# Kernel tuning notes

Hardware: AMD Instinct MI355X
Metric: run time of the kernel (lower is better)

## Reference

```python
import jax, jax.numpy as jnp
import numpy as np

B, K, T, C = 4, 8, 2048, 64

def setup_inputs() -> dict:
    key = jax.random.key(0)
    ks = jax.random.split(key, 7)
    return {
        "x": jax.random.normal(ks[0], (B, K, T, C), dtype=jnp.float32),
        "Wq": jax.random.normal(ks[1], (C, C), dtype=jnp.float32) / np.sqrt(C),
        "bq": jax.random.normal(ks[2], (C,), dtype=jnp.float32) * 0.01,
        "Wk": jax.random.normal(ks[3], (C, C), dtype=jnp.float32) / np.sqrt(C),
        "bk": jax.random.normal(ks[4], (C,), dtype=jnp.float32) * 0.01,
        "Wv": jax.random.normal(ks[5], (C, C), dtype=jnp.float32) / np.sqrt(C),
        "bv": jax.random.normal(ks[6], (C,), dtype=jnp.float32) * 0.01,
    }

def reference(x, Wq, bq, Wk, bk, Wv, bv):
    c_dim = x.shape[-1]
    # torch nn.Linear: y = x @ W.T + b
    q = jnp.einsum('bktc,dc->bktd', x, Wq) + bq
    k = jnp.einsum('bktc,dc->bktd', x, Wk) + bk
    v = jnp.einsum('bktc,dc->bktd', x, Wv) + bv
    scores = jnp.einsum('bkic,bkjc->bkij', q, k) / jnp.sqrt(jnp.float32(c_dim))
    attn = jax.nn.softmax(scores, axis=-1)
    out = jnp.einsum('bkij,bkjc->bkic', attn, v)
    return out
```

## Files before the change

### kernel.cpp

```cpp
#include <hip/hip_runtime.h>


#define T_DIM 2048
#define NHEAD 32
#define HSTRIDE (T_DIM * 64)
#define QSCALE 0.18033688011112042f
#define SOFF  8.0f

#define SWZ(row, grp) ((row) * 64 + ((((grp) ^ ((row) & 7)) & 7) * 8))

#define RAW_BARRIER() asm volatile("s_waitcnt lgkmcnt(0)\n\ts_barrier" ::: "memory")

typedef _Float16 h8 __attribute__((ext_vector_type(8)));
typedef _Float16 h4 __attribute__((ext_vector_type(4)));
typedef __fp16   g2 __attribute__((ext_vector_type(2)));
typedef float    f4 __attribute__((ext_vector_type(4)));
typedef float    fv16 __attribute__((ext_vector_type(16)));

union H4U { h4 v; g2 p[2]; };
union H8U { h8 v; h4 h[2]; g2 p[4]; };

#if defined(__has_builtin)
#if __has_builtin(__builtin_amdgcn_exp2f)
#define EXP2(x) __builtin_amdgcn_exp2f(x)
#endif
#endif
#ifndef EXP2
__device__ inline float exp2_raw(float x) {
    float r;
    asm("v_exp_f32 %0, %1" : "=v"(r) : "v"(x));
    return r;
}
#define EXP2(x) exp2_raw(x)
#endif

__device__ inline h4 cvt4(f4 x) {
    H4U u;
    u.p[0] = __builtin_amdgcn_cvt_pkrtz(x[0], x[1]);
    u.p[1] = __builtin_amdgcn_cvt_pkrtz(x[2], x[3]);
    return u.v;
}

__device__ inline h8 cvt8(f4 a, f4 b) {
    H8U r;
    r.h[0] = cvt4(a);
    r.h[1] = cvt4(b);
    return r.v;
}

__device__ inline fv16 splat16(float x) {
    fv16 r;
    #pragma unroll
    for (int i = 0; i < 16; ++i) r[i] = x;
    return r;
}

__global__ __launch_bounds__(256) void qkv_proj_kernel(
    const float* __restrict__ x,
    const float* __restrict__ Wq, const float* __restrict__ bq,
    const float* __restrict__ Wk, const float* __restrict__ bk,
    const float* __restrict__ Wv, const float* __restrict__ bv,
    _Float16* __restrict__ qh, _Float16* __restrict__ khT,
    _Float16* __restrict__ vtT)
{
    __shared__ _Float16 ws[3][64 * 64];
    __shared__ _Float16 ot[64 * 64];
    __shared__ float bsh[3][64];

    const int tid  = threadIdx.x;
    const int row0 = blockIdx.x * 64;
    const int head = blockIdx.x >> 5;
    const int t0   = (blockIdx.x & 31) * 64;

    #pragma unroll
    for (int m = 0; m < 3; ++m) {
        const float* Wm = (m == 0) ? Wq : ((m == 1) ? Wk : Wv);
        const float* bm = (m == 0) ? bq : ((m == 1) ? bk : bv);
        #pragma unroll
        for (int pass = 0; pass < 4; ++pass) {
            const int idx = pass * 1024 + tid * 4;
            const int d = idx >> 6, c = idx & 63;
            f4 wv = *(const f4*)(Wm + idx);
            *(h4*)&ws[m][SWZ(d, c >> 3) + (c & 7)] = cvt4(wv);
        }
        if (tid < 64) bsh[m][tid] = bm[tid];
    }

    const int w    = tid >> 6;
    const int lane = tid & 63;
    const int l15  = lane & 15;
    const int qd   = lane >> 4;

    h8 af[2];
    {
        const float* xp = x + (size_t)(row0 + w * 16 + l15) * 64 + qd * 8;
        #pragma unroll
        for (int ch = 0; ch < 2; ++ch) {
            f4 a0 = *(const f4*)(xp + ch * 32);
            f4 a1 = *(const f4*)(xp + ch * 32 + 4);
            af[ch] = cvt8(a0, a1);
        }
    }
    __syncthreads();

    #pragma unroll
    for (int m = 0; m < 3; ++m) {
        h8 bf[4][2];
        #pragma unroll
        for (int ns = 0; ns < 4; ++ns)
            #pragma unroll
            for (int ch = 0; ch < 2; ++ch)
                bf[ns][ch] = *(const h8*)&ws[m][SWZ(ns * 16 + l15, ch * 4 + qd)];

        f4 acc[4];
        #pragma unroll
        for (int ns = 0; ns < 4; ++ns)
            acc[ns] = (f4){0.f, 0.f, 0.f, 0.f};
        #pragma unroll
        for (int ch = 0; ch < 2; ++ch)
            #pragma unroll
            for (int ns = 0; ns < 4; ++ns)
                acc[ns] = __builtin_amdgcn_mfma_f32_16x16x32_f16(
                    af[ch], bf[ns][ch], acc[ns], 0, 0, 0);

        __syncthreads();
        if (m < 2) {
            #pragma unroll
            for (int ns = 0; ns < 4; ++ns) {
                const int d = ns * 16 + l15;
                const float bias = bsh[m][d];
                #pragma unroll
                for (int r = 0; r < 4; ++r) {
                    const int t = w * 16 + qd * 4 + r;
                    float v = acc[ns][r] + bias;
                    if (m == 0) v *= QSCALE;
                    ot[SWZ(t, d >> 3) + (d & 7)] = (_Float16)v;
                }
            }
            __syncthreads();
            if (m == 0) {
                #pragma unroll
                for (int pass = 0; pass < 2; ++pass) {
                    const int t  = pass * 32 + (tid >> 3);
                    const int c0 = (tid & 7) * 8;
                    *(h8*)&qh[(size_t)(row0 + t) * 64 + c0] =
                        *(const h8*)&ot[SWZ(t, tid & 7)];
                }
            } else {
                #pragma unroll
                for (int pass = 0; pass < 2; ++pass) {
                    const int f   = pass * 2048 + tid * 8;
                    const int kb  = f >> 11;
                    const int cs  = (f >> 9) & 3;
                    const int l   = (f >> 3) & 63;
                    const int p   = l & 31;
                    const int w16 = p & 15;
                    const int sw  = ((w16 & 12) == 4) ? (w16 + 4)
                                  : (((w16 & 12) == 8) ? (w16 - 4) : w16);
                    const int tact = kb * 32 + (p & 16) + sw;
                    const int g8   = cs * 2 + (l >> 5);
                    *(h8*)&khT[(size_t)head * HSTRIDE + (t0 >> 6) * 4096 + f] =
                        *(const h8*)&ot[SWZ(tact, g8)];
                }
            }
        } else {
            #pragma unroll
            for (int ns = 0; ns < 4; ++ns) {
                const int d = ns * 16 + l15;
                const float bias = bsh[2][d];
                const int tl = w * 16 + qd * 4;
                f4 pvf;
                #pragma unroll
                for (int r = 0; r < 4; ++r)
                    pvf[r] = acc[ns][r] + bias;
                *(h4*)&ot[SWZ(d, tl >> 3) + (tl & 7)] = cvt4(pvf);
            }
            __syncthreads();
            #pragma unroll
            for (int pass = 0; pass < 2; ++pass) {
                const int f  = pass * 2048 + tid * 8;
                const int q2 = f >> 9;
                const int b  = q2 >> 1, cc = q2 & 1;
                const int l  = (f >> 3) & 63;
                const int c  = cc * 32 + (l & 31);
                const int tg = b * 2 + (l >> 5);
                *(h8*)&vtT[(size_t)head * HSTRIDE + (t0 >> 6) * 4096 + f] =
                    *(const h8*)&ot[SWZ(c, tg)];
            }
        }
    }
}

__global__ __launch_bounds__(384, 2) void attn_kernel(
    const _Float16* __restrict__ qh, const _Float16* __restrict__ khT,
    const _Float16* __restrict__ vtT, float* __restrict__ out)
{
    __shared__ _Float16 tiles[3][8192];
    const int tid  = threadIdx.x;
    const int w    = tid >> 6;
    const int lane = tid & 63;

    const int bid  = blockIdx.x;
    const int xcd  = bid & 7;
    const int slot = bid >> 3;
    const int head = xcd * 4 + (slot >> 3);
    const int qpart = slot & 7;

    if (w < 4) {
        const int q0  = qpart * 256 + w * 64;
        const int l31 = lane & 31;
        const int lh  = lane >> 5;

        h8 qf[2][4];
        #pragma unroll
        for (int qs = 0; qs < 2; ++qs) {
            const _Float16* qp = qh + (size_t)(head * T_DIM + q0 + qs * 32 + l31) * 64 + lh * 8;
            #pragma unroll
            for (int cs = 0; cs < 4; ++cs)
                qf[qs][cs] = *(const h8*)(qp + cs * 16);
        }

        f4 rs4[2] = {(f4){0.f,0.f,0.f,0.f}, (f4){0.f,0.f,0.f,0.f}};
        fv16 oacc[2][2];
        #pragma unroll
        for (int qs = 0; qs < 2; ++qs)
            #pragma unroll
            for (int cc = 0; cc < 2; ++cc)
                oacc[qs][cc] = splat16(0.f);

        const int ko = lane * 8;
        const _Float16* c0 = &tiles[0][0];
        const _Float16* c1 = &tiles[1][0];
        const _Float16* c2 = &tiles[2][0];

        __syncthreads();

        fv16 st[2][2];
        {
            h8 kf[2][4];
            #pragma unroll
            for (int kb = 0; kb < 2; ++kb)
                #pragma unroll
                for (int cs = 0; cs < 4; ++cs)
                    kf[kb][cs] = *(const h8*)(c0 + kb * 2048 + cs * 512 + ko);
            #pragma unroll
            for (int kb = 0; kb < 2; ++kb)
                #pragma unroll
                for (int qs = 0; qs < 2; ++qs)
                    st[kb][qs] = splat16(-SOFF);
            #pragma unroll
            for (int cs = 0; cs < 4; ++cs)
                #pragma unroll
                for (int kb = 0; kb < 2; ++kb)
                    #pragma unroll
                    for (int qs = 0; qs < 2; ++qs)
                        st[kb][qs] = __builtin_amdgcn_mfma_f32_32x32x16_f16(
                            kf[kb][cs], qf[qs][cs], st[kb][qs], 0, 0, 0);
        }

        for (int it = 0; it < 32; ++it) {
            h8 kf[2][4];
            if (it < 31) {
                #pragma unroll
                for (int kb = 0; kb < 2; ++kb)
                    #pragma unroll
                    for (int cs = 0; cs < 4; ++cs)
                        kf[kb][cs] = *(const h8*)(c1 + kb * 2048 + cs * 512 + ko);
            }
            h8 vf[4][2];
            #pragma unroll
            for (int b = 0; b < 4; ++b)
                #pragma unroll
                for (int cc = 0; cc < 2; ++cc)
                    vf[b][cc] = *(const h8*)(c0 + 4096 + (b * 2 + cc) * 512 + ko);

            #pragma unroll
            for (int qs = 0; qs < 2; ++qs) {
                H8U pa[4];
                #pragma unroll
                for (int kb = 0; kb < 2; ++kb)
                    #pragma unroll
                    for (int g = 0; g < 4; ++g) {
                        f4 p;
                        p[0] = EXP2(st[kb][qs][4 * g + 0]);
                        p[1] = EXP2(st[kb][qs][4 * g + 1]);
                        p[2] = EXP2(st[kb][qs][4 * g + 2]);
                        p[3] = EXP2(st[kb][qs][4 * g + 3]);
                        rs4[qs] += p;
                        const int b = kb * 2 + (g >> 1);
                        pa[b].p[(g & 1) * 2 + 0] = __builtin_amdgcn_cvt_pkrtz(p[0], p[1]);
                        pa[b].p[(g & 1) * 2 + 1] = __builtin_amdgcn_cvt_pkrtz(p[2], p[3]);
                    }
                #pragma unroll
                for (int b = 0; b < 4; ++b)
                    #pragma unroll
                    for (int cc = 0; cc < 2; ++cc)
                        oacc[qs][cc] = __builtin_amdgcn_mfma_f32_32x32x16_f16(
                            pa[b].v, vf[b][cc], oacc[qs][cc], 0, 0, 0);
            }

            if (it < 31) {
                #pragma unroll
                for (int kb = 0; kb < 2; ++kb)
                    #pragma unroll
                    for (int qs = 0; qs < 2; ++qs)
                        st[kb][qs] = splat16(-SOFF);
                #pragma unroll
                for (int cs = 0; cs < 4; ++cs)
                    #pragma unroll
                    for (int kb = 0; kb < 2; ++kb)
                        #pragma unroll
                        for (int qs = 0; qs < 2; ++qs)
                            st[kb][qs] = __builtin_amdgcn_mfma_f32_32x32x16_f16(
                                kf[kb][cs], qf[qs][cs], st[kb][qs], 0, 0, 0);
            }

            const _Float16* tmp = c0; c0 = c1; c1 = c2; c2 = tmp;
            __syncthreads();
        }

        #pragma unroll
        for (int qs = 0; qs < 2; ++qs) {
            float lsum = (rs4[qs][0] + rs4[qs][1]) + (rs4[qs][2] + rs4[qs][3]);
            lsum += __shfl_xor(lsum, 32, 64);
            const float linv = 1.f / lsum;
            #pragma unroll
            for (int r = 0; r < 16; ++r) {
                const int qrow = (r & 3) + 8 * (r >> 2) + 4 * lh;
                const float fac = __shfl(linv, qrow, 64);
                #pragma unroll
                for (int cc = 0; cc < 2; ++cc)
                    out[(size_t)(head * T_DIM + q0 + qs * 32 + qrow) * 64 + cc * 32 + l31] =
                        oacc[qs][cc][r] * fac;
            }
        }
    } else {
        const _Float16* src = ((w == 4) ? khT : vtT) + (size_t)head * HSTRIDE;
        const int off = (w - 4) * 4096;
        _Float16* d0 = &tiles[0][off];
        _Float16* d1 = &tiles[1][off];
        _Float16* d2 = &tiles[2][off];
        const int lo = lane * 8;
        h8 sA[8], sB[8];

        #pragma unroll
        for (int b = 0; b < 8; ++b) sA[b] = *(const h8*)(src + b * 512 + lo);
        #pragma unroll
        for (int b = 0; b < 8; ++b) sB[b] = *(const h8*)(src + 4096 + b * 512 + lo);
        #pragma unroll
        for (int b = 0; b < 8; ++b) *(h8*)(d0 + b * 512 + lo) = sA[b];
        #pragma unroll
        for (int b = 0; b < 8; ++b) *(h8*)(d1 + b * 512 + lo) = sB[b];
        #pragma unroll
        for (int b = 0; b < 8; ++b) sA[b] = *(const h8*)(src + 8192 + b * 512 + lo);
        const _Float16* sp = src + 3 * 4096;
        RAW_BARRIER();

        _Float16* w0 = d2;
        _Float16* w1 = d0;
        _Float16* w2 = d1;

        for (int t2 = 0; t2 < 16; ++t2) {
            if (t2 < 15) {
                #pragma unroll
                for (int b = 0; b < 8; ++b) sB[b] = *(const h8*)(sp + b * 512 + lo);
                sp += 4096;
                #pragma unroll
                for (int b = 0; b < 8; ++b) *(h8*)(w0 + b * 512 + lo) = sA[b];
            }
            RAW_BARRIER();
            { _Float16* t = w0; w0 = w1; w1 = w2; w2 = t; }
            if (t2 < 14) {
                #pragma unroll
                for (int b = 0; b < 8; ++b) sA[b] = *(const h8*)(sp + b * 512 + lo);
                sp += 4096;
            }
            if (t2 < 15) {
                #pragma unroll
                for (int b = 0; b < 8; ++b) *(h8*)(w0 + b * 512 + lo) = sB[b];
            }
            RAW_BARRIER();
            { _Float16* t = w0; w0 = w1; w1 = w2; w2 = t; }
        }
    }
}

extern "C" void kernel_launch(void* const* d_in, const int* in_sizes, int n_in,
                              void* d_out, int out_size, void* d_ws, size_t ws_size,
                              hipStream_t stream)
{
    (void)in_sizes; (void)n_in; (void)out_size; (void)ws_size;
    const float* x  = (const float*)d_in[0];
    const float* Wq = (const float*)d_in[1];
    const float* bq = (const float*)d_in[2];
    const float* Wk = (const float*)d_in[3];
    const float* bk = (const float*)d_in[4];
    const float* Wv = (const float*)d_in[5];
    const float* bv = (const float*)d_in[6];
    float* out = (float*)d_out;

    _Float16* qh  = (_Float16*)d_ws;
    _Float16* khT = qh + (size_t)NHEAD * HSTRIDE;
    _Float16* vtT = khT + (size_t)NHEAD * HSTRIDE;

    hipLaunchKernelGGL(qkv_proj_kernel, dim3(1024), dim3(256), 0, stream,
                       x, Wq, bq, Wk, bk, Wv, bv, qh, khT, vtT);
    hipLaunchKernelGGL(attn_kernel, dim3(256), dim3(384), 0, stream,
                       qh, khT, vtT, out);
}
```

Baseline: 124.9 us.

## Halve attention consumer warps per block, double grid, restructure projection epilogue

The attention kernel now uses 2 consumer warps plus 2 loader warps per block (256 threads) and launches 512 blocks, each covering 128 query rows instead of 256. This spreads the work over more blocks and gives more overlap across the CUs. The cost is that each block streams K/V tiles for half as many queries, which doubles total K/V tile traffic. The inner loop now loads K fragments per key block just before use, which lowers register pressure, and raises wave priority with s_setprio around the MFMA section. The projection kernel issues the x loads before the weight staging, reuses the weight LDS as output staging, and collapses the per-matrix barriers into two.

New measurement: 136.8 us. +9.5%, slower.

```diff
diff --git a/kernel.cpp b/kernel.cpp
--- a/kernel.cpp
+++ b/kernel.cpp
@@ -64,13 +64,27 @@
     _Float16* __restrict__ vtT)
 {
     __shared__ _Float16 ws[3][64 * 64];
-    __shared__ _Float16 ot[64 * 64];
     __shared__ float bsh[3][64];
 
     const int tid  = threadIdx.x;
     const int row0 = blockIdx.x * 64;
     const int head = blockIdx.x >> 5;
     const int t0   = (blockIdx.x & 31) * 64;
+
+    const int w    = tid >> 6;
+    const int lane = tid & 63;
+    const int l15  = lane & 15;
+    const int qd   = lane >> 4;
+
+    f4 xa[2][2];
+    {
+        const float* xp = x + (size_t)(row0 + w * 16 + l15) * 64 + qd * 8;
+        #pragma unroll
+        for (int ch = 0; ch < 2; ++ch) {
+            xa[ch][0] = *(const f4*)(xp + ch * 32);
+            xa[ch][1] = *(const f4*)(xp + ch * 32 + 4);
+        }
+    }
 
     #pragma unroll
     for (int m = 0; m < 3; ++m) {
@@ -86,23 +100,14 @@
         if (tid < 64) bsh[m][tid] = bm[tid];
     }
 
-    const int w    = tid >> 6;
-    const int lane = tid & 63;
-    const int l15  = lane & 15;
-    const int qd   = lane >> 4;
-
     h8 af[2];
-    {
-        const float* xp = x + (size_t)(row0 + w * 16 + l15) * 64 + qd * 8;
-        #pragma unroll
-        for (int ch = 0; ch < 2; ++ch) {
-            f4 a0 = *(const f4*)(xp + ch * 32);
-            f4 a1 = *(const f4*)(xp + ch * 32 + 4);
-            af[ch] = cvt8(a0, a1);
-        }
-    }
+    #pragma unroll
+    for (int ch = 0; ch < 2; ++ch)
+        af[ch] = cvt8(xa[ch][0], xa[ch][1]);
+
     __syncthreads();
 
+    f4 acc[3][4];
     #pragma unroll
     for (int m = 0; m < 3; ++m) {
         h8 bf[4][2];
@@ -111,87 +116,84 @@
             #pragma unroll
             for (int ch = 0; ch < 2; ++ch)
                 bf[ns][ch] = *(const h8*)&ws[m][SWZ(ns * 16 + l15, ch * 4 + qd)];
-
-        f4 acc[4];
         #pragma unroll
         for (int ns = 0; ns < 4; ++ns)
-            acc[ns] = (f4){0.f, 0.f, 0.f, 0.f};
+            acc[m][ns] = (f4){0.f, 0.f, 0.f, 0.f};
         #pragma unroll
         for (int ch = 0; ch < 2; ++ch)
             #pragma unroll
             for (int ns = 0; ns < 4; ++ns)
-                acc[ns] = __builtin_amdgcn_mfma_f32_16x16x32_f16(
-                    af[ch], bf[ns][ch], acc[ns], 0, 0, 0);
-
-        __syncthreads();
-        if (m < 2) {
-            #pragma unroll
-            for (int ns = 0; ns < 4; ++ns) {
-                const int d = ns * 16 + l15;
-                const float bias = bsh[m][d];
-                #pragma unroll
-                for (int r = 0; r < 4; ++r) {
-                    const int t = w * 16 + qd * 4 + r;
-                    float v = acc[ns][r] + bias;
-                    if (m == 0) v *= QSCALE;
-                    ot[SWZ(t, d >> 3) + (d & 7)] = (_Float16)v;
-                }
-            }
-            __syncthreads();
-            if (m == 0) {
-                #pragma unroll
-                for (int pass = 0; pass < 2; ++pass) {
-                    const int t  = pass * 32 + (tid >> 3);
-                    const int c0 = (tid & 7) * 8;
-                    *(h8*)&qh[(size_t)(row0 + t) * 64 + c0] =
-                        *(const h8*)&ot[SWZ(t, tid & 7)];
-                }
-            } else {
-                #pragma unroll
-                for (int pass = 0; pass < 2; ++pass) {
-                    const int f   = pass * 2048 + tid * 8;
-                    const int kb  = f >> 11;
-                    const int cs  = (f >> 9) & 3;
-                    const int l   = (f >> 3) & 63;
-                    const int p   = l & 31;
-                    const int w16 = p & 15;
-                    const int sw  = ((w16 & 12) == 4) ? (w16 + 4)
-                                  : (((w16 & 12) == 8) ? (w16 - 4) : w16);
-                    const int tact = kb * 32 + (p & 16) + sw;
-                    const int g8   = cs * 2 + (l >> 5);
-                    *(h8*)&khT[(size_t)head * HSTRIDE + (t0 >> 6) * 4096 + f] =
-                        *(const h8*)&ot[SWZ(tact, g8)];
-                }
-            }
-        } else {
-            #pragma unroll
-            for (int ns = 0; ns < 4; ++ns) {
-                const int d = ns * 16 + l15;
-                const float bias = bsh[2][d];
-                const int tl = w * 16 + qd * 4;
-                f4 pvf;
-                #pragma unroll
-                for (int r = 0; r < 4; ++r)
-                    pvf[r] = acc[ns][r] + bias;
-                *(h4*)&ot[SWZ(d, tl >> 3) + (tl & 7)] = cvt4(pvf);
-            }
-            __syncthreads();
-            #pragma unroll
-            for (int pass = 0; pass < 2; ++pass) {
-                const int f  = pass * 2048 + tid * 8;
-                const int q2 = f >> 9;
-                const int b  = q2 >> 1, cc = q2 & 1;
-                const int l  = (f >> 3) & 63;
-                const int c  = cc * 32 + (l & 31);
-                const int tg = b * 2 + (l >> 5);
-                *(h8*)&vtT[(size_t)head * HSTRIDE + (t0 >> 6) * 4096 + f] =
-                    *(const h8*)&ot[SWZ(c, tg)];
-            }
-        }
-    }
-}
-
-__global__ __launch_bounds__(384, 2) void attn_kernel(
+                acc[m][ns] = __builtin_amdgcn_mfma_f32_16x16x32_f16(
+                    af[ch], bf[ns][ch], acc[m][ns], 0, 0, 0);
+    }
+
+    __syncthreads();
+
+    #pragma unroll
+    for (int m = 0; m < 2; ++m) {
+        #pragma unroll
+        for (int ns = 0; ns < 4; ++ns) {
+            const int d = ns * 16 + l15;
+            const float bias = bsh[m][d];
+            #pragma unroll
+            for (int r = 0; r < 4; ++r) {
+                const int t = w * 16 + qd * 4 + r;
+                float v = acc[m][ns][r] + bias;
+                if (m == 0) v *= QSCALE;
+                ws[m][SWZ(t, d >> 3) + (d & 7)] = (_Float16)v;
+            }
+        }
+    }
+    #pragma unroll
+    for (int ns = 0; ns < 4; ++ns) {
+        const int d = ns * 16 + l15;
+        const float bias = bsh[2][d];
+        const int tl = w * 16 + qd * 4;
+        f4 pvf;
+        #pragma unroll
+        for (int r = 0; r < 4; ++r)
+            pvf[r] = acc[2][ns][r] + bias;
+        *(h4*)&ws[2][SWZ(d, tl >> 3) + (tl & 7)] = cvt4(pvf);
+    }
+
+    __syncthreads();
+
+    #pragma unroll
+    for (int pass = 0; pass < 2; ++pass) {
+        const int t  = pass * 32 + (tid >> 3);
+        const int c0 = (tid & 7) * 8;
+        *(h8*)&qh[(size_t)(row0 + t) * 64 + c0] =
+            *(const h8*)&ws[0][SWZ(t, tid & 7)];
+    }
+    #pragma unroll
+    for (int pass = 0; pass < 2; ++pass) {
+        const int f   = pass * 2048 + tid * 8;
+        const int kb  = f >> 11;
+        const int cs  = (f >> 9) & 3;
+        const int l   = (f >> 3) & 63;
+        const int p   = l & 31;
+        const int w16 = p & 15;
+        const int sw  = ((w16 & 12) == 4) ? (w16 + 4)
+                      : (((w16 & 12) == 8) ? (w16 - 4) : w16);
+        const int tact = kb * 32 + (p & 16) + sw;
+        const int g8   = cs * 2 + (l >> 5);
+        *(h8*)&khT[(size_t)head * HSTRIDE + (t0 >> 6) * 4096 + f] =
+            *(const h8*)&ws[1][SWZ(tact, g8)];
+    }
+    #pragma unroll
+    for (int pass = 0; pass < 2; ++pass) {
+        const int f  = pass * 2048 + tid * 8;
+        const int q2 = f >> 9;
+        const int b  = q2 >> 1, cc = q2 & 1;
+        const int l  = (f >> 3) & 63;
+        const int c  = cc * 32 + (l & 31);
+        const int tg = b * 2 + (l >> 5);
+        *(h8*)&vtT[(size_t)head * HSTRIDE + (t0 >> 6) * 4096 + f] =
+            *(const h8*)&ws[2][SWZ(c, tg)];
+    }
+}
+
+__global__ __launch_bounds__(256, 2) void attn_kernel(
     const _Float16* __restrict__ qh, const _Float16* __restrict__ khT,
     const _Float16* __restrict__ vtT, float* __restrict__ out)
 {
@@ -203,11 +205,11 @@
     const int bid  = blockIdx.x;
     const int xcd  = bid & 7;
     const int slot = bid >> 3;
-    const int head = xcd * 4 + (slot >> 3);
-    const int qpart = slot & 7;
-
-    if (w < 4) {
-        const int q0  = qpart * 256 + w * 64;
+    const int head = xcd * 4 + (slot >> 4);
+    const int qpart = slot & 15;
+
+    if (w < 2) {
+        const int q0  = qpart * 128 + w * 64;
         const int l31 = lane & 31;
         const int lh  = lane >> 5;
 
@@ -236,37 +238,23 @@
         __syncthreads();
 
         fv16 st[2][2];
-        {
-            h8 kf[2][4];
-            #pragma unroll
-            for (int kb = 0; kb < 2; ++kb)
-                #pragma unroll
-                for (int cs = 0; cs < 4; ++cs)
-                    kf[kb][cs] = *(const h8*)(c0 + kb * 2048 + cs * 512 + ko);
-            #pragma unroll
-            for (int kb = 0; kb < 2; ++kb)
+        #pragma unroll
+        for (int kb = 0; kb < 2; ++kb) {
+            h8 kf[4];
+            #pragma unroll
+            for (int cs = 0; cs < 4; ++cs)
+                kf[cs] = *(const h8*)(c0 + kb * 2048 + cs * 512 + ko);
+            st[kb][0] = splat16(-SOFF);
+            st[kb][1] = splat16(-SOFF);
+            #pragma unroll
+            for (int cs = 0; cs < 4; ++cs)
                 #pragma unroll
                 for (int qs = 0; qs < 2; ++qs)
-                    st[kb][qs] = splat16(-SOFF);
-            #pragma unroll
-            for (int cs = 0; cs < 4; ++cs)
-                #pragma unroll
-                for (int kb = 0; kb < 2; ++kb)
-                    #pragma unroll
-                    for (int qs = 0; qs < 2; ++qs)
-                        st[kb][qs] = __builtin_amdgcn_mfma_f32_32x32x16_f16(
-                            kf[kb][cs], qf[qs][cs], st[kb][qs], 0, 0, 0);
+                    st[kb][qs] = __builtin_amdgcn_mfma_f32_32x32x16_f16(
+                        kf[cs], qf[qs][cs], st[kb][qs], 0, 0, 0);
         }
 
         for (int it = 0; it < 32; ++it) {
-            h8 kf[2][4];
-            if (it < 31) {
-                #pragma unroll
-                for (int kb = 0; kb < 2; ++kb)
-                    #pragma unroll
-                    for (int cs = 0; cs < 4; ++cs)
-                        kf[kb][cs] = *(const h8*)(c1 + kb * 2048 + cs * 512 + ko);
-            }
             h8 vf[4][2];
             #pragma unroll
             for (int b = 0; b < 4; ++b)
@@ -274,11 +262,13 @@
                 for (int cc = 0; cc < 2; ++cc)
                     vf[b][cc] = *(const h8*)(c0 + 4096 + (b * 2 + cc) * 512 + ko);
 
-            #pragma unroll
-            for (int qs = 0; qs < 2; ++qs) {
-                H8U pa[4];
-                #pragma unroll
-                for (int kb = 0; kb < 2; ++kb)
+            __builtin_amdgcn_s_setprio(1);
+
+            #pragma unroll
+            for (int qs = 0; qs < 2; ++qs)
+                #pragma unroll
+                for (int kb = 0; kb < 2; ++kb) {
+                    H8U pa[2];
                     #pragma unroll
                     for (int g = 0; g < 4; ++g) {
                         f4 p;
@@ -287,33 +277,38 @@
                         p[2] = EXP2(st[kb][qs][4 * g + 2]);
                         p[3] = EXP2(st[kb][qs][4 * g + 3]);
                         rs4[qs] += p;
-                        const int b = kb * 2 + (g >> 1);
-                        pa[b].p[(g & 1) * 2 + 0] = __builtin_amdgcn_cvt_pkrtz(p[0], p[1]);
-                        pa[b].p[(g & 1) * 2 + 1] = __builtin_amdgcn_cvt_pkrtz(p[2], p[3]);
+                        pa[g >> 1].p[(g & 1) * 2 + 0] = __builtin_amdgcn_cvt_pkrtz(p[0], p[1]);
+                        pa[g >> 1].p[(g & 1) * 2 + 1] = __builtin_amdgcn_cvt_pkrtz(p[2], p[3]);
                     }
-                #pragma unroll
-                for (int b = 0; b < 4; ++b)
                     #pragma unroll
-                    for (int cc = 0; cc < 2; ++cc)
-                        oacc[qs][cc] = __builtin_amdgcn_mfma_f32_32x32x16_f16(
-                            pa[b].v, vf[b][cc], oacc[qs][cc], 0, 0, 0);
-            }
+                    for (int bl = 0; bl < 2; ++bl) {
+                        const int b = kb * 2 + bl;
+                        #pragma unroll
+                        for (int cc = 0; cc < 2; ++cc)
+                            oacc[qs][cc] = __builtin_amdgcn_mfma_f32_32x32x16_f16(
+                                pa[bl].v, vf[b][cc], oacc[qs][cc], 0, 0, 0);
+                    }
+                }
 
             if (it < 31) {
                 #pragma unroll
-                for (int kb = 0; kb < 2; ++kb)
+                for (int kb = 0; kb < 2; ++kb) {
+                    h8 kf[4];
                     #pragma unroll
-                    for (int qs = 0; qs < 2; ++qs)
-                        st[kb][qs] = splat16(-SOFF);
-                #pragma unroll
-                for (int cs = 0; cs < 4; ++cs)
+                    for (int cs = 0; cs < 4; ++cs)
+                        kf[cs] = *(const h8*)(c1 + kb * 2048 + cs * 512 + ko);
+                    st[kb][0] = splat16(-SOFF);
+                    st[kb][1] = splat16(-SOFF);
                     #pragma unroll
-                    for (int kb = 0; kb < 2; ++kb)
+                    for (int cs = 0; cs < 4; ++cs)
                         #pragma unroll
                         for (int qs = 0; qs < 2; ++qs)
                             st[kb][qs] = __builtin_amdgcn_mfma_f32_32x32x16_f16(
-                                kf[kb][cs], qf[qs][cs], st[kb][qs], 0, 0, 0);
-            }
+                                kf[cs], qf[qs][cs], st[kb][qs], 0, 0, 0);
+                }
+            }
+
+            __builtin_amdgcn_s_setprio(0);
 
             const _Float16* tmp = c0; c0 = c1; c1 = c2; c2 = tmp;
             __syncthreads();
@@ -335,8 +330,8 @@
             }
         }
     } else {
-        const _Float16* src = ((w == 4) ? khT : vtT) + (size_t)head * HSTRIDE;
-        const int off = (w - 4) * 4096;
+        const _Float16* src = ((w == 2) ? khT : vtT) + (size_t)head * HSTRIDE;
+        const int off = (w - 2) * 4096;
         _Float16* d0 = &tiles[0][off];
         _Float16* d1 = &tiles[1][off];
         _Float16* d2 = &tiles[2][off];
@@ -405,6 +400,6 @@
 
     hipLaunchKernelGGL(qkv_proj_kernel, dim3(1024), dim3(256), 0, stream,
                        x, Wq, bq, Wk, bk, Wv, bv, qh, khT, vtT);
-    hipLaunchKernelGGL(attn_kernel, dim3(256), dim3(384), 0, stream,
+    hipLaunchKernelGGL(attn_kernel, dim3(512), dim3(256), 0, stream,
                        qh, khT, vtT, out);
 }
```
